# Kernel optimization log

Measured on AMD Instinct MI355X. Metric: run time of the kernel, lower is better.

## Reference

```python
import jax, jax.numpy as jnp
import numpy as np

N = 100000
E = 1600000
D_IN = 128
D_HID = 128

def setup_inputs() -> dict:
    key = jax.random.key(0)
    ks = jax.random.split(key, 8)
    x = jax.random.normal(ks[0], (N, D_IN), dtype=jnp.float32)
    edge_index = jax.random.randint(ks[1], (2, E), 0, N, dtype=jnp.int32)
    edge_weight = jax.random.uniform(ks[2], (E,), dtype=jnp.float32)
    W1 = jax.random.normal(ks[3], (D_IN, D_HID), dtype=jnp.float32) / np.sqrt(D_IN)
    b1 = jnp.zeros((D_HID,), dtype=jnp.float32)
    W2 = jax.random.normal(ks[4], (D_HID, D_HID), dtype=jnp.float32) / np.sqrt(D_HID)
    b2 = jnp.zeros((D_HID,), dtype=jnp.float32)
    W3 = jax.random.normal(ks[5], (D_HID, 1), dtype=jnp.float32) / np.sqrt(D_HID)
    b3 = jnp.zeros((1,), dtype=jnp.float32)
    return {"x": x, "edge_index": edge_index, "edge_weight": edge_weight,
            "W1": W1, "b1": b1, "W2": W2, "b2": b2, "W3": W3, "b3": b3}

def _gcn_norm(edge_index, edge_weight, n):
    # Add self-loops (weight 1) and compute symmetric normalization, as in PyG GCNConv.
    loop = jnp.arange(n, dtype=edge_index.dtype)
    src = jnp.concatenate([edge_index[0], loop])
    dst = jnp.concatenate([edge_index[1], loop])
    w = jnp.concatenate([edge_weight, jnp.ones((n,), edge_weight.dtype)])
    deg = jax.ops.segment_sum(w, dst, num_segments=n)  # [N]
    dis = jnp.where(deg > 0, jax.lax.rsqrt(jnp.where(deg > 0, deg, 1.0)), 0.0)
    norm = dis[src] * w * dis[dst]  # [E+N]
    return src, dst, norm

def _gcn_conv(x, W, b, src, dst, norm, n):
    h = x @ W  # [N, out]
    msg = norm[:, None] * h[src]  # gather + scale, [E+N, out]
    out = jax.ops.segment_sum(msg, dst, num_segments=n)  # scatter-add
    return out + b

def reference(x, edge_index, edge_weight, W1, b1, W2, b2, W3, b3):
    n = x.shape[0]
    src, dst, norm = _gcn_norm(edge_index, edge_weight, n)
    h = jax.nn.relu(_gcn_conv(x, W1, b1, src, dst, norm, n))
    h = jax.nn.relu(_gcn_conv(h, W2, b2, src, dst, norm, n))
    h = _gcn_conv(h, W3, b3, src, dst, norm, n)
    return jax.nn.relu(h).squeeze(-1)  # [N]
```

## Files before the change

### kernel.cpp

```cpp
#include <hip/hip_runtime.h>
#include <hip/hip_fp16.h>
#include <math.h>

#define NFEAT 128
#define CAP 64
#define BINSHIFT 7
#define GB 256

typedef int2 EdgeRec;

__device__ inline float4 h4_to_f4(uint2 u) {
  __half2 lo = *(__half2*)&u.x;
  __half2 hi = *(__half2*)&u.y;
  float2 a = __half22float2(lo), b = __half22float2(hi);
  return make_float4(a.x, a.y, b.x, b.y);
}
__device__ inline uint2 f4_to_h4(float4 v) {
  __half2 lo = __floats2half2_rn(v.x, v.y);
  __half2 hi = __floats2half2_rn(v.z, v.w);
  uint2 r; r.x = *(unsigned*)&lo; r.y = *(unsigned*)&hi; return r;
}


__global__ __launch_bounds__(256) void k_hist(const int* __restrict__ dst,
                                              unsigned* __restrict__ histG,
                                              int E, int EPB, int nbins) {
  __shared__ unsigned lh[1024];
  for (int i = threadIdx.x; i < nbins; i += 256) lh[i] = 0;
  __syncthreads();
  int start = blockIdx.x * EPB;
  int end = start + EPB; if (end > E) end = E;
  for (int e = start + threadIdx.x; e < end; e += 256)
    atomicAdd(&lh[dst[e] >> BINSHIFT], 1u);
  __syncthreads();
  for (int i = threadIdx.x; i < nbins; i += 256)
    histG[(size_t)i * GB + blockIdx.x] = lh[i];
}

__global__ __launch_bounds__(256) void k_scanT(const unsigned* __restrict__ histG,
                                               unsigned* __restrict__ binTot, int nbins) {
  int wave = threadIdx.x >> 6;
  int lane = threadIdx.x & 63;
  int bin = blockIdx.x * 4 + wave;
  if (bin >= nbins) return;
  uint4 v = *(const uint4*)(histG + (size_t)bin * GB + lane * 4);
  int s = (int)(v.x + v.y + v.z + v.w);
#pragma unroll
  for (int off = 32; off > 0; off >>= 1) s += __shfl_down(s, off, 64);
  if (lane == 0) binTot[bin] = (unsigned)s;
}

__global__ __launch_bounds__(1024) void k_scanB(const unsigned* __restrict__ binTot,
                                                unsigned* __restrict__ binBase, int nbins) {
  __shared__ unsigned tot[1024];
  int b = threadIdx.x;
  tot[b] = (b < nbins) ? binTot[b] : 0;
  __syncthreads();
  for (int off = 1; off < 1024; off <<= 1) {
    unsigned v = (b >= off) ? tot[b - off] : 0;
    __syncthreads();
    tot[b] += v;
    __syncthreads();
  }
  if (b < nbins) binBase[b] = (b == 0) ? 0u : tot[b - 1];
  if (b == 0) binBase[nbins] = tot[1023];
}

__global__ __launch_bounds__(256) void k_scanC(unsigned* __restrict__ histG,
                                               const unsigned* __restrict__ binBase,
                                               int nbins) {
  int wave = threadIdx.x >> 6;
  int lane = threadIdx.x & 63;
  int bin = blockIdx.x * 4 + wave;
  if (bin >= nbins) return;
  uint4 v = *(const uint4*)(histG + (size_t)bin * GB + lane * 4);
  unsigned i1 = v.x + v.y;
  unsigned i2 = i1 + v.z;
  unsigned i3 = i2 + v.w;
  int inc = (int)i3;
#pragma unroll
  for (int off = 1; off < 64; off <<= 1) {
    int t = __shfl_up(inc, off, 64);
    if (lane >= off) inc += t;
  }
  unsigned base = binBase[bin] + (unsigned)inc - i3;
  uint4 o;
  o.x = base;
  o.y = base + v.x;
  o.z = base + i1;
  o.w = base + i2;
  *(uint4*)(histG + (size_t)bin * GB + lane * 4) = o;
}

__global__ __launch_bounds__(256) void k_scatter(const int* __restrict__ src,
                                                 const int* __restrict__ dst,
                                                 const float* __restrict__ ew,
                                                 const unsigned* __restrict__ histG,
                                                 uint2* __restrict__ sorted,
                                                 int E, int EPB, int nbins) {
  __shared__ unsigned lrank[1024];
  __shared__ unsigned lbase[1024];
  for (int i = threadIdx.x; i < nbins; i += 256) {
    lrank[i] = 0;
    lbase[i] = histG[(size_t)i * GB + blockIdx.x];
  }
  __syncthreads();
  int start = blockIdx.x * EPB;
  int end = start + EPB; if (end > E) end = E;
  for (int e = start + threadIdx.x; e < end; e += 256) {
    int d = dst[e];
    int bin = d >> BINSHIFT;
    unsigned r = atomicAdd(&lrank[bin], 1u);
    uint2 rec;
    rec.x = (unsigned)src[e] | ((unsigned)(d & 127) << 24);
    rec.y = __float_as_uint(ew[e]);
    sorted[lbase[bin] + r] = rec;
  }
}

__global__ __launch_bounds__(256) void k_csr(const uint2* __restrict__ sorted,
                                             const unsigned* __restrict__ binBase,
                                             unsigned* __restrict__ cnt,
                                             EdgeRec* __restrict__ ep,
                                             float* __restrict__ dis, int N) {
  int bin = blockIdx.x;
  __shared__ unsigned lcnt[128];
  __shared__ float lsum[128];
  if (threadIdx.x < 128) { lcnt[threadIdx.x] = 0; lsum[threadIdx.x] = 0.f; }
  __syncthreads();
  unsigned s0 = binBase[bin], s1 = binBase[bin + 1];
  int node0 = bin << BINSHIFT;
  for (unsigned e = s0 + threadIdx.x; e < s1; e += 256) {
    uint2 rec = sorted[e];
    int dlow = rec.x >> 24;
    int srcn = rec.x & 0xFFFFFF;
    unsigned slot = atomicAdd(&lcnt[dlow], 1u);
    EdgeRec r; r.x = srcn; r.y = (int)rec.y;
    ep[(size_t)(node0 + dlow) * CAP + slot] = r;
    atomicAdd(&lsum[dlow], __uint_as_float(rec.y));
  }
  __syncthreads();
  if (threadIdx.x < 128) {
    int node = node0 + threadIdx.x;
    if (node < N) {
      cnt[node] = lcnt[threadIdx.x];
      dis[node] = 1.0f / sqrtf(1.0f + lsum[threadIdx.x]);
    }
  }
}

__global__ __launch_bounds__(256) void k_premul(EdgeRec* __restrict__ ep,
                                                const unsigned* __restrict__ cnt,
                                                const float* __restrict__ dis, int N) {
  int wave = threadIdx.x >> 6;
  int lane = threadIdx.x & 63;
  int node = blockIdx.x * 4 + wave;
  if (node >= N) return;
  int c = (int)cnt[node];
  if (lane < c) {
    int e = node * CAP + lane;
    EdgeRec r = ep[e];
    r.y = __float_as_int(dis[r.x] * __int_as_float(r.y));
    ep[e] = r;
  }
}


__global__ __launch_bounds__(1024) void k_gemm1(const float* __restrict__ X,
                                                const float* __restrict__ W,
                                                __half* __restrict__ Y,
                                                int N, int numTiles) {
  __shared__ float sW[128 * 128];
  __shared__ float sX[128 * 128];
  int t = threadIdx.x;
  int wave = __builtin_amdgcn_readfirstlane(t >> 6);
  int lane = t & 63;
  int lr = (lane >> 3) & 7;
  int lc = lane & 7;
  int wr = wave >> 2;
  int wc = wave & 3;

  {
    const float4* W4 = (const float4*)W;
    float4* sW4 = (float4*)sW;
    for (int i = t; i < 4096; i += 1024) sW4[i] = W4[i];
  }

  const float4* X4 = (const float4*)X;
  int grmax = N - 1;
  int r0 = wr * 32 + lr * 4;
  int c0 = wc * 32 + lc * 4;
  int swzk = ((r0 >> 2) & 7) << 2;

  for (int tile = blockIdx.x; tile < numTiles; tile += gridDim.x) {
    int rowBase = tile * 128;
    __syncthreads();
    {
      int kg = t & 31;
      int rb = t >> 5;
#pragma unroll
      for (int p = 0; p < 4; p++) {
        int r = rb + 32 * p;
        int gr = rowBase + r; if (gr > grmax) gr = grmax;
        float4 v = X4[(size_t)gr * 32 + kg];
        int swz = ((r >> 2) & 7) << 2;
        *(float4*)(&sX[r * 128 + ((kg * 4) ^ swz)]) = v;
      }
    }
    __syncthreads();

    float4 acc[4];
#pragma unroll
    for (int i = 0; i < 4; i++) acc[i] = make_float4(0.f, 0.f, 0.f, 0.f);

#pragma unroll 1
    for (int kg = 0; kg < 32; kg++) {
      int kk0 = kg * 4;
      float4 xf[4];
#pragma unroll
      for (int i = 0; i < 4; i++)
        xf[i] = *(const float4*)(&sX[(r0 + i) * 128 + (kk0 ^ swzk)]);
      float4 wf[4];
#pragma unroll
      for (int kk = 0; kk < 4; kk++)
        wf[kk] = *(const float4*)(&sW[(kk0 + kk) * 128 + c0]);
#pragma unroll
      for (int kk = 0; kk < 4; kk++) {
#pragma unroll
        for (int i = 0; i < 4; i++) {
          float xs = (&xf[i].x)[kk];
          acc[i].x = fmaf(xs, wf[kk].x, acc[i].x);
          acc[i].y = fmaf(xs, wf[kk].y, acc[i].y);
          acc[i].z = fmaf(xs, wf[kk].z, acc[i].z);
          acc[i].w = fmaf(xs, wf[kk].w, acc[i].w);
        }
      }
    }

#pragma unroll
    for (int i = 0; i < 4; i++) {
      int row = rowBase + r0 + i;
      if (row < N)
        *(uint2*)(Y + (size_t)row * 128 + c0) = f4_to_h4(acc[i]);
    }
  }
}


__global__ __launch_bounds__(1024) void k_aggemm(const __half* __restrict__ H,
                                                 const unsigned* __restrict__ cntA,
                                                 const EdgeRec* __restrict__ ep,
                                                 const float* __restrict__ dis,
                                                 const float* __restrict__ bias,
                                                 const float* __restrict__ Wm,
                                                 __half* __restrict__ Y,
                                                 int N, int numTiles) {
  __shared__ float sW[128 * 128];
  __shared__ float sX[2][64 * 128];
  int t = threadIdx.x;
  int wave = __builtin_amdgcn_readfirstlane(t >> 6);
  int lane = t & 63;

  {
    const float4* W4 = (const float4*)Wm;
    float4* sW4 = (float4*)sW;
    for (int i = t; i < 4096; i += 1024) sW4[i] = W4[i];
  }
  __syncthreads();

  int gw = wave;
  int half = lane >> 5;
  int l32 = lane & 31;
  int mw = wave - 12;
  int wr = (mw >> 1) & 1;
  int wc = mw & 1;
  int lr = (lane >> 3) & 7;
  int lc = lane & 7;
  int rB = wr * 32 + lr * 4;
  int cA = wc * 64 + lc * 4;
  int cB = cA + 32;
  int swzm = lr << 2;
  int s2b = 2 * gw;

  for (int it = 0;; it++) {
    int gtile = blockIdx.x + it * gridDim.x;
    int mtile = gtile - (int)gridDim.x;
    bool anyG = gtile < numTiles;
    bool anyM = (it >= 1) && (mtile < numTiles);
    if (!anyG && !anyM) break;

    if (wave < 12) {
      if (anyG) {
        float* buf = sX[it & 1];
        int tileBase = gtile * 64;
        int cnts[3];
#pragma unroll
        for (int k = 0; k < 3; k++) {
          int s2 = s2b + 24 * k;
          int node = tileBase + s2 + half;
          int nodec = node < N ? node : N - 1;
          unsigned pk = cntA[nodec];
          cnts[k] = (s2 < 64 && node < N) ? (int)pk : 0;
        }
#pragma unroll 1
        for (int k = 0; k < 3; k++) {
          int s2 = s2b + 24 * k;
          if (s2 >= 64) break;
          int node = tileBase + s2 + half;
          int cnt = cnts[k];
          int beg = (node < N ? node : 0) * CAP;
          int last = beg + cnt - 1;

          float4 acc = make_float4(0.f, 0.f, 0.f, 0.f);
          if (cnt > 0) {
            EdgeRec e0[4], e1[4], e2[4], e3[4];
            uint2 h0[4], h1[4];
#pragma unroll
            for (int q = 0; q < 4; q++) { int e = beg + q;     e0[q] = ep[e <= last ? e : last]; }
#pragma unroll
            for (int q = 0; q < 4; q++) { int e = beg + 4 + q; e1[q] = ep[e <= last ? e : last]; }
#pragma unroll
            for (int q = 0; q < 4; q++) { int e = beg + 8 + q; e2[q] = ep[e <= last ? e : last]; }
#pragma unroll
            for (int q = 0; q < 4; q++)
              h0[q] = *(const uint2*)(H + (size_t)e0[q].x * 128 + 4 * l32);
#pragma unroll
            for (int q = 0; q < 4; q++)
              h1[q] = *(const uint2*)(H + (size_t)e1[q].x * 128 + 4 * l32);
            for (int p = 0; p < cnt; p += 4) {
              uint2 h2[4];
#pragma unroll
              for (int q = 0; q < 4; q++) {
                int e = beg + p + 12 + q;
                e3[q] = ep[e <= last ? e : last];
              }
#pragma unroll
              for (int q = 0; q < 4; q++)
                h2[q] = *(const uint2*)(H + (size_t)e2[q].x * 128 + 4 * l32);
#pragma unroll
              for (int q = 0; q < 4; q++) {
                float w = (p + q < cnt) ? __int_as_float(e0[q].y) : 0.f;
                float4 hv = h4_to_f4(h0[q]);
                acc.x = fmaf(w, hv.x, acc.x);
                acc.y = fmaf(w, hv.y, acc.y);
                acc.z = fmaf(w, hv.z, acc.z);
                acc.w = fmaf(w, hv.w, acc.w);
              }
#pragma unroll
              for (int q = 0; q < 4; q++) {
                e0[q] = e1[q]; e1[q] = e2[q]; e2[q] = e3[q];
                h0[q] = h1[q]; h1[q] = h2[q];
              }
            }
          }
          if (node < N) {
            float ds = dis[node];
            float4 hn = h4_to_f4(*(const uint2*)(H + (size_t)node * 128 + 4 * l32));
            acc.x = fmaf(ds, hn.x, acc.x);
            acc.y = fmaf(ds, hn.y, acc.y);
            acc.z = fmaf(ds, hn.z, acc.z);
            acc.w = fmaf(ds, hn.w, acc.w);
            float4 bv = *(const float4*)(bias + 4 * l32);
            float4 o;
            o.x = fmaf(ds, acc.x, bv.x); o.x = o.x > 0.f ? o.x : 0.f;
            o.y = fmaf(ds, acc.y, bv.y); o.y = o.y > 0.f ? o.y : 0.f;
            o.z = fmaf(ds, acc.z, bv.z); o.z = o.z > 0.f ? o.z : 0.f;
            o.w = fmaf(ds, acc.w, bv.w); o.w = o.w > 0.f ? o.w : 0.f;
            int s = s2 + half;
            int swz = ((s >> 2) & 7) << 2;
            *(float4*)(&buf[s * 128 + ((4 * l32) ^ swz)]) = o;
          }
        }
      }
    } else {
      if (anyM) {
        const float* buf = sX[(it - 1) & 1];
        float4 accA[4], accB[4];
#pragma unroll
        for (int i = 0; i < 4; i++) {
          accA[i] = make_float4(0.f, 0.f, 0.f, 0.f);
          accB[i] = make_float4(0.f, 0.f, 0.f, 0.f);
        }
#pragma unroll 2
        for (int kg = 0; kg < 32; kg++) {
          int kk0 = kg * 4;
          float4 xf[4];
#pragma unroll
          for (int i = 0; i < 4; i++)
            xf[i] = *(const float4*)(&buf[(rB + i) * 128 + (kk0 ^ swzm)]);
#pragma unroll
          for (int kk = 0; kk < 4; kk++) {
            float4 wA = *(const float4*)(&sW[(kk0 + kk) * 128 + cA]);
            float4 wB = *(const float4*)(&sW[(kk0 + kk) * 128 + cB]);
#pragma unroll
            for (int i = 0; i < 4; i++) {
              float xs = (&xf[i].x)[kk];
              accA[i].x = fmaf(xs, wA.x, accA[i].x);
              accA[i].y = fmaf(xs, wA.y, accA[i].y);
              accA[i].z = fmaf(xs, wA.z, accA[i].z);
              accA[i].w = fmaf(xs, wA.w, accA[i].w);
              accB[i].x = fmaf(xs, wB.x, accB[i].x);
              accB[i].y = fmaf(xs, wB.y, accB[i].y);
              accB[i].z = fmaf(xs, wB.z, accB[i].z);
              accB[i].w = fmaf(xs, wB.w, accB[i].w);
            }
          }
        }
        int rowBase = mtile * 64;
#pragma unroll
        for (int i = 0; i < 4; i++) {
          int row = rowBase + rB + i;
          if (row < N) {
            *(uint2*)(Y + (size_t)row * 128 + cA) = f4_to_h4(accA[i]);
            *(uint2*)(Y + (size_t)row * 128 + cB) = f4_to_h4(accB[i]);
          }
        }
      }
    }
    __syncthreads();
  }
}


__global__ __launch_bounds__(256) void k_agg_final(const __half* __restrict__ H,
                                                   const unsigned* __restrict__ cntA,
                                                   const EdgeRec* __restrict__ ep,
                                                   const float* __restrict__ dis,
                                                   const float* __restrict__ bias,
                                                   const float* __restrict__ W3,
                                                   float* __restrict__ z, int N) {
  int wave = __builtin_amdgcn_readfirstlane(threadIdx.x >> 6);
  int lane = threadIdx.x & 63;
  int half = lane >> 5;
  int l32  = lane & 31;
  int node = blockIdx.x * 8 + wave * 2 + half;
  int nodec = node < N ? node : N - 1;
  int cnt = (node < N) ? (int)cntA[nodec] : 0;
  int beg = nodec * CAP;
  int last = beg + cnt - 1;

  float4 acc = make_float4(0.f, 0.f, 0.f, 0.f);
  if (cnt > 0) {
    EdgeRec e0[4], e1[4], e2[4];
    uint2 h0[4], h1[4];
#pragma unroll
    for (int q = 0; q < 4; q++) { int e = beg + q;     e0[q] = ep[e <= last ? e : last]; }
#pragma unroll
    for (int q = 0; q < 4; q++) { int e = beg + 4 + q; e1[q] = ep[e <= last ? e : last]; }
#pragma unroll
    for (int q = 0; q < 4; q++)
      h0[q] = *(const uint2*)(H + (size_t)e0[q].x * 128 + 4 * l32);
    for (int p = 0; p < cnt; p += 4) {
      uint2 h1n[4];
#pragma unroll
      for (int q = 0; q < 4; q++) {
        int e = beg + p + 8 + q;
        e2[q] = ep[e <= last ? e : last];
      }
#pragma unroll
      for (int q = 0; q < 4; q++)
        h1n[q] = *(const uint2*)(H + (size_t)e1[q].x * 128 + 4 * l32);
#pragma unroll
      for (int q = 0; q < 4; q++) {
        float w = (p + q < cnt) ? __int_as_float(e0[q].y) : 0.f;
        float4 hv = h4_to_f4(h0[q]);
        acc.x = fmaf(w, hv.x, acc.x);
        acc.y = fmaf(w, hv.y, acc.y);
        acc.z = fmaf(w, hv.z, acc.z);
        acc.w = fmaf(w, hv.w, acc.w);
      }
#pragma unroll
      for (int q = 0; q < 4; q++) { e0[q] = e1[q]; e1[q] = e2[q]; h0[q] = h1n[q]; }
    }
  }
  float ds = dis[nodec];
  float4 hn = h4_to_f4(*(const uint2*)(H + (size_t)nodec * 128 + 4 * l32));
  acc.x = fmaf(ds, hn.x, acc.x);
  acc.y = fmaf(ds, hn.y, acc.y);
  acc.z = fmaf(ds, hn.z, acc.z);
  acc.w = fmaf(ds, hn.w, acc.w);
  float4 bv = *(const float4*)(bias + 4 * l32);
  float4 w3v = *(const float4*)(W3 + 4 * l32);
  float o, pdot = 0.f;
  o = fmaf(ds, acc.x, bv.x); o = o > 0.f ? o : 0.f; pdot = fmaf(o, w3v.x, pdot);
  o = fmaf(ds, acc.y, bv.y); o = o > 0.f ? o : 0.f; pdot = fmaf(o, w3v.y, pdot);
  o = fmaf(ds, acc.z, bv.z); o = o > 0.f ? o : 0.f; pdot = fmaf(o, w3v.z, pdot);
  o = fmaf(ds, acc.w, bv.w); o = o > 0.f ? o : 0.f; pdot = fmaf(o, w3v.w, pdot);
#pragma unroll
  for (int off = 16; off > 0; off >>= 1) pdot += __shfl_down(pdot, off, 32);
  if (l32 == 0 && node < N) z[node] = pdot;
}


__global__ void k_aggs(const float* __restrict__ z, const unsigned* __restrict__ cntA,
                       const EdgeRec* __restrict__ ep, const float* __restrict__ dis,
                       const float* __restrict__ b3, float* __restrict__ out, int N) {
  int n = blockIdx.x * blockDim.x + threadIdx.x;
  if (n >= N) return;
  int cnt = (int)cntA[n];
  float dsn = dis[n];
  float acc = dsn * z[n];
  int beg = n * CAP;
#pragma unroll 4
  for (int e = beg; e < beg + cnt; e++) {
    EdgeRec p = ep[e];
    acc = fmaf(__int_as_float(p.y), z[p.x], acc);
  }
  acc = fmaf(dsn, acc, b3[0]);
  out[n] = acc > 0.f ? acc : 0.f;
}


extern "C" void kernel_launch(void* const* d_in, const int* in_sizes, int n_in,
                              void* d_out, int out_size, void* d_ws, size_t ws_size,
                              hipStream_t stream) {
  const float* x  = (const float*)d_in[0];
  const int*   ei = (const int*)d_in[1];
  const float* ew = (const float*)d_in[2];
  const float* W1 = (const float*)d_in[3];
  const float* b1 = (const float*)d_in[4];
  const float* W2 = (const float*)d_in[5];
  const float* b2 = (const float*)d_in[6];
  const float* W3 = (const float*)d_in[7];
  const float* b3 = (const float*)d_in[8];
  int N = in_sizes[0] / NFEAT;
  int E = in_sizes[2];
  const int* srcp = ei;
  const int* dstp = ei + E;

  char* p = (char*)d_ws;
  auto carve = [&](size_t bytes) -> void* {
    void* r = (void*)p;
    p += (bytes + 511) & ~(size_t)511;
    return r;
  };
  int nbins = (N + 127) >> BINSHIFT;
  unsigned* cnt     = (unsigned*)carve(sizeof(unsigned) * N);
  float*    dis     = (float*)carve(sizeof(float) * N);
  EdgeRec*  ep      = (EdgeRec*)carve(sizeof(EdgeRec) * (size_t)N * CAP);
  __half*   t1      = (__half*)carve(sizeof(__half) * (size_t)N * NFEAT);
  __half*   t2      = (__half*)carve(sizeof(__half) * (size_t)N * NFEAT);
  float*    z       = (float*)carve(sizeof(float) * N);
  unsigned* histG   = (unsigned*)carve(sizeof(unsigned) * (size_t)GB * nbins);
  unsigned* binTot  = (unsigned*)carve(sizeof(unsigned) * nbins);
  unsigned* binBase = (unsigned*)carve(sizeof(unsigned) * (nbins + 1));
  uint2*    sorted  = (uint2*)carve(sizeof(uint2) * (size_t)E);

  int gN = (N + 255) / 256;
  int numTiles128 = (N + 127) / 128;
  int numTiles64  = (N + 63) / 64;
  int GG = 256;
  int EPB = (E + GB - 1) / GB;
  int gS = (nbins + 3) / 4;
  int gP = (N + 3) / 4;
  int gF = (N + 7) / 8;

  k_hist<<<GB, 256, 0, stream>>>(dstp, histG, E, EPB, nbins);
  k_scanT<<<gS, 256, 0, stream>>>(histG, binTot, nbins);
  k_scanB<<<1, 1024, 0, stream>>>(binTot, binBase, nbins);
  k_scanC<<<gS, 256, 0, stream>>>(histG, binBase, nbins);
  k_scatter<<<GB, 256, 0, stream>>>(srcp, dstp, ew, histG, sorted, E, EPB, nbins);
  k_csr<<<nbins, 256, 0, stream>>>(sorted, binBase, cnt, ep, dis, N);
  k_gemm1<<<GG, 1024, 0, stream>>>(x, W1, t1, N, numTiles128);
  k_premul<<<gP, 256, 0, stream>>>(ep, cnt, dis, N);
  k_aggemm<<<GG, 1024, 0, stream>>>(t1, cnt, ep, dis, b1, W2, t2, N, numTiles64);
  k_agg_final<<<gF, 256, 0, stream>>>(t2, cnt, ep, dis, b2, W3, z, N);
  k_aggs<<<gN, 256, 0, stream>>>(z, cnt, ep, dis, b3, (float*)d_out, N);
}
```

Baseline: 430.7 us.

## Split each node's edge list across both wave halves and zero-pad CSR slots

The aggregation in k_aggemm and k_agg_final now gives each node one full wave instead of one half-wave. Each 32-lane half handles alternate edges, and the halves combine their partial sums with a cross-half shuffle. k_csr now zero-fills the unused slots in each node's fixed-capacity edge block so the loops can read padded entries safely without per-edge masking, and it clamps counts at CAP. This doubles the memory-level parallelism per node and lowers the per-wave edge-chain latency. The costs are extra zero-fill writes (about N*CAP records) during CSR construction, reduced work per wave, and a changed launch grid for the final aggregation.

```diff
diff --git a/kernel.cpp b/kernel.cpp
--- a/kernel.cpp
+++ b/kernel.cpp
@@ -135,15 +135,28 @@
     int dlow = rec.x >> 24;
     int srcn = rec.x & 0xFFFFFF;
     unsigned slot = atomicAdd(&lcnt[dlow], 1u);
-    EdgeRec r; r.x = srcn; r.y = (int)rec.y;
-    ep[(size_t)(node0 + dlow) * CAP + slot] = r;
+    if (slot < CAP) {
+      EdgeRec r; r.x = srcn; r.y = (int)rec.y;
+      ep[(size_t)(node0 + dlow) * CAP + slot] = r;
+    }
     atomicAdd(&lsum[dlow], __uint_as_float(rec.y));
   }
   __syncthreads();
+  for (int i = threadIdx.x; i < 128 * CAP; i += 256) {
+    int dlow = i >> 6;
+    int slot = i & (CAP - 1);
+    int node = node0 + dlow;
+    unsigned c = lcnt[dlow]; if (c > CAP) c = CAP;
+    if (node < N && (unsigned)slot >= c) {
+      EdgeRec zr; zr.x = 0; zr.y = 0;
+      ep[(size_t)node * CAP + slot] = zr;
+    }
+  }
   if (threadIdx.x < 128) {
     int node = node0 + threadIdx.x;
     if (node < N) {
-      cnt[node] = lcnt[threadIdx.x];
+      unsigned c = lcnt[threadIdx.x]; if (c > CAP) c = CAP;
+      cnt[node] = c;
       dis[node] = 1.0f / sqrtf(1.0f + lsum[threadIdx.x]);
     }
   }
@@ -269,7 +282,7 @@
   __syncthreads();
 
   int gw = wave;
-  int half = lane >> 5;
+  int hi = lane >> 5;
   int l32 = lane & 31;
   int mw = wave - 12;
   int wr = (mw >> 1) & 1;
@@ -280,7 +293,6 @@
   int cA = wc * 64 + lc * 4;
   int cB = cA + 32;
   int swzm = lr << 2;
-  int s2b = 2 * gw;
 
   for (int it = 0;; it++) {
     int gtile = blockIdx.x + it * gridDim.x;
@@ -293,67 +305,56 @@
       if (anyG) {
         float* buf = sX[it & 1];
         int tileBase = gtile * 64;
-        int cnts[3];
-#pragma unroll
-        for (int k = 0; k < 3; k++) {
-          int s2 = s2b + 24 * k;
-          int node = tileBase + s2 + half;
-          int nodec = node < N ? node : N - 1;
-          unsigned pk = cntA[nodec];
-          cnts[k] = (s2 < 64 && node < N) ? (int)pk : 0;
-        }
-#pragma unroll 1
-        for (int k = 0; k < 3; k++) {
-          int s2 = s2b + 24 * k;
-          if (s2 >= 64) break;
-          int node = tileBase + s2 + half;
-          int cnt = cnts[k];
-          int beg = (node < N ? node : 0) * CAP;
-          int last = beg + cnt - 1;
+        for (int s = gw; s < 64; s += 12) {
+          int node = tileBase + s;
+          if (node >= N) continue;
+          int cnt = (int)cntA[node];
+          int beg = node * CAP;
+          int emax = beg + CAP - 1;
 
           float4 acc = make_float4(0.f, 0.f, 0.f, 0.f);
           if (cnt > 0) {
-            EdgeRec e0[4], e1[4], e2[4], e3[4];
-            uint2 h0[4], h1[4];
-#pragma unroll
-            for (int q = 0; q < 4; q++) { int e = beg + q;     e0[q] = ep[e <= last ? e : last]; }
-#pragma unroll
-            for (int q = 0; q < 4; q++) { int e = beg + 4 + q; e1[q] = ep[e <= last ? e : last]; }
-#pragma unroll
-            for (int q = 0; q < 4; q++) { int e = beg + 8 + q; e2[q] = ep[e <= last ? e : last]; }
-#pragma unroll
-            for (int q = 0; q < 4; q++)
-              h0[q] = *(const uint2*)(H + (size_t)e0[q].x * 128 + 4 * l32);
-#pragma unroll
-            for (int q = 0; q < 4; q++)
-              h1[q] = *(const uint2*)(H + (size_t)e1[q].x * 128 + 4 * l32);
+            EdgeRec e0[4], e1[4];
+            uint2 hA0, hB0;
+#define LDE(d_, idx_) { int q_ = beg + (idx_); q_ = q_ <= emax ? q_ : emax; d_ = ep[q_]; }
+            LDE(e0[0], 0) LDE(e0[1], 1) LDE(e0[2], 2) LDE(e0[3], 3)
+            LDE(e1[0], 4) LDE(e1[1], 5) LDE(e1[2], 6) LDE(e1[3], 7)
+            {
+              int sA = hi ? e0[1].x : e0[0].x;
+              int sB = hi ? e0[3].x : e0[2].x;
+              hA0 = *(const uint2*)(H + (size_t)sA * 128 + 4 * l32);
+              hB0 = *(const uint2*)(H + (size_t)sB * 128 + 4 * l32);
+            }
             for (int p = 0; p < cnt; p += 4) {
-              uint2 h2[4];
-#pragma unroll
-              for (int q = 0; q < 4; q++) {
-                int e = beg + p + 12 + q;
-                e3[q] = ep[e <= last ? e : last];
-              }
-#pragma unroll
-              for (int q = 0; q < 4; q++)
-                h2[q] = *(const uint2*)(H + (size_t)e2[q].x * 128 + 4 * l32);
-#pragma unroll
-              for (int q = 0; q < 4; q++) {
-                float w = (p + q < cnt) ? __int_as_float(e0[q].y) : 0.f;
-                float4 hv = h4_to_f4(h0[q]);
-                acc.x = fmaf(w, hv.x, acc.x);
-                acc.y = fmaf(w, hv.y, acc.y);
-                acc.z = fmaf(w, hv.z, acc.z);
-                acc.w = fmaf(w, hv.w, acc.w);
-              }
-#pragma unroll
-              for (int q = 0; q < 4; q++) {
-                e0[q] = e1[q]; e1[q] = e2[q]; e2[q] = e3[q];
-                h0[q] = h1[q]; h1[q] = h2[q];
-              }
+              EdgeRec e2[4];
+              LDE(e2[0], p + 8) LDE(e2[1], p + 9) LDE(e2[2], p + 10) LDE(e2[3], p + 11)
+              int nA = hi ? e1[1].x : e1[0].x;
+              int nB = hi ? e1[3].x : e1[2].x;
+              uint2 hA1 = *(const uint2*)(H + (size_t)nA * 128 + 4 * l32);
+              uint2 hB1 = *(const uint2*)(H + (size_t)nB * 128 + 4 * l32);
+              float wA = __int_as_float(hi ? e0[1].y : e0[0].y);
+              float wB = __int_as_float(hi ? e0[3].y : e0[2].y);
+              float4 a = h4_to_f4(hA0);
+              float4 b = h4_to_f4(hB0);
+              acc.x = fmaf(wA, a.x, acc.x);
+              acc.y = fmaf(wA, a.y, acc.y);
+              acc.z = fmaf(wA, a.z, acc.z);
+              acc.w = fmaf(wA, a.w, acc.w);
+              acc.x = fmaf(wB, b.x, acc.x);
+              acc.y = fmaf(wB, b.y, acc.y);
+              acc.z = fmaf(wB, b.z, acc.z);
+              acc.w = fmaf(wB, b.w, acc.w);
+#pragma unroll
+              for (int q = 0; q < 4; q++) { e0[q] = e1[q]; e1[q] = e2[q]; }
+              hA0 = hA1; hB0 = hB1;
             }
+#undef LDE
           }
-          if (node < N) {
+          acc.x += __shfl_xor(acc.x, 32, 64);
+          acc.y += __shfl_xor(acc.y, 32, 64);
+          acc.z += __shfl_xor(acc.z, 32, 64);
+          acc.w += __shfl_xor(acc.w, 32, 64);
+          if (hi == 0) {
             float ds = dis[node];
             float4 hn = h4_to_f4(*(const uint2*)(H + (size_t)node * 128 + 4 * l32));
             acc.x = fmaf(ds, hn.x, acc.x);
@@ -366,7 +367,6 @@
             o.y = fmaf(ds, acc.y, bv.y); o.y = o.y > 0.f ? o.y : 0.f;
             o.z = fmaf(ds, acc.z, bv.z); o.z = o.z > 0.f ? o.z : 0.f;
             o.w = fmaf(ds, acc.w, bv.w); o.w = o.w > 0.f ? o.w : 0.f;
-            int s = s2 + half;
             int swz = ((s >> 2) & 7) << 2;
             *(float4*)(&buf[s * 128 + ((4 * l32) ^ swz)]) = o;
           }
@@ -431,64 +431,74 @@
                                                    float* __restrict__ z, int N) {
   int wave = __builtin_amdgcn_readfirstlane(threadIdx.x >> 6);
   int lane = threadIdx.x & 63;
-  int half = lane >> 5;
-  int l32  = lane & 31;
-  int node = blockIdx.x * 8 + wave * 2 + half;
-  int nodec = node < N ? node : N - 1;
-  int cnt = (node < N) ? (int)cntA[nodec] : 0;
-  int beg = nodec * CAP;
-  int last = beg + cnt - 1;
+  int hi = lane >> 5;
+  int l32 = lane & 31;
+  int node = blockIdx.x * 4 + wave;
+  if (node >= N) return;
+  int cnt = (int)cntA[node];
+  int beg = node * CAP;
+  int emax = beg + CAP - 1;
 
   float4 acc = make_float4(0.f, 0.f, 0.f, 0.f);
   if (cnt > 0) {
-    EdgeRec e0[4], e1[4], e2[4];
-    uint2 h0[4], h1[4];
-#pragma unroll
-    for (int q = 0; q < 4; q++) { int e = beg + q;     e0[q] = ep[e <= last ? e : last]; }
-#pragma unroll
-    for (int q = 0; q < 4; q++) { int e = beg + 4 + q; e1[q] = ep[e <= last ? e : last]; }
-#pragma unroll
-    for (int q = 0; q < 4; q++)
-      h0[q] = *(const uint2*)(H + (size_t)e0[q].x * 128 + 4 * l32);
+    EdgeRec e0[4], e1[4];
+    uint2 hA0, hB0;
+#define LDE(d_, idx_) { int q_ = beg + (idx_); q_ = q_ <= emax ? q_ : emax; d_ = ep[q_]; }
+    LDE(e0[0], 0) LDE(e0[1], 1) LDE(e0[2], 2) LDE(e0[3], 3)
+    LDE(e1[0], 4) LDE(e1[1], 5) LDE(e1[2], 6) LDE(e1[3], 7)
+    {
+      int sA = hi ? e0[1].x : e0[0].x;
+      int sB = hi ? e0[3].x : e0[2].x;
+      hA0 = *(const uint2*)(H + (size_t)sA * 128 + 4 * l32);
+      hB0 = *(const uint2*)(H + (size_t)sB * 128 + 4 * l32);
+    }
     for (int p = 0; p < cnt; p += 4) {
-      uint2 h1n[4];
-#pragma unroll
-      for (int q = 0; q < 4; q++) {
-        int e = beg + p + 8 + q;
-        e2[q] = ep[e <= last ? e : last];
-      }
-#pragma unroll
-      for (int q = 0; q < 4; q++)
-        h1n[q] = *(const uint2*)(H + (size_t)e1[q].x * 128 + 4 * l32);
-#pragma unroll
-      for (int q = 0; q < 4; q++) {
-        float w = (p + q < cnt) ? __int_as_float(e0[q].y) : 0.f;
-        float4 hv = h4_to_f4(h0[q]);
-        acc.x = fmaf(w, hv.x, acc.x);
-        acc.y = fmaf(w, hv.y, acc.y);
-        acc.z = fmaf(w, hv.z, acc.z);
-        acc.w = fmaf(w, hv.w, acc.w);
-      }
-#pragma unroll
-      for (int q = 0; q < 4; q++) { e0[q] = e1[q]; e1[q] = e2[q]; h0[q] = h1n[q]; }
-    }
-  }
-  float ds = dis[nodec];
-  float4 hn = h4_to_f4(*(const uint2*)(H + (size_t)nodec * 128 + 4 * l32));
-  acc.x = fmaf(ds, hn.x, acc.x);
-  acc.y = fmaf(ds, hn.y, acc.y);
-  acc.z = fmaf(ds, hn.z, acc.z);
-  acc.w = fmaf(ds, hn.w, acc.w);
-  float4 bv = *(const float4*)(bias + 4 * l32);
-  float4 w3v = *(const float4*)(W3 + 4 * l32);
-  float o, pdot = 0.f;
-  o = fmaf(ds, acc.x, bv.x); o = o > 0.f ? o : 0.f; pdot = fmaf(o, w3v.x, pdot);
-  o = fmaf(ds, acc.y, bv.y); o = o > 0.f ? o : 0.f; pdot = fmaf(o, w3v.y, pdot);
-  o = fmaf(ds, acc.z, bv.z); o = o > 0.f ? o : 0.f; pdot = fmaf(o, w3v.z, pdot);
-  o = fmaf(ds, acc.w, bv.w); o = o > 0.f ? o : 0.f; pdot = fmaf(o, w3v.w, pdot);
-#pragma unroll
-  for (int off = 16; off > 0; off >>= 1) pdot += __shfl_down(pdot, off, 32);
-  if (l32 == 0 && node < N) z[node] = pdot;
+      EdgeRec e2[4];
+      LDE(e2[0], p + 8) LDE(e2[1], p + 9) LDE(e2[2], p + 10) LDE(e2[3], p + 11)
+      int nA = hi ? e1[1].x : e1[0].x;
+      int nB = hi ? e1[3].x : e1[2].x;
+      uint2 hA1 = *(const uint2*)(H + (size_t)nA * 128 + 4 * l32);
+      uint2 hB1 = *(const uint2*)(H + (size_t)nB * 128 + 4 * l32);
+      float wA = __int_as_float(hi ? e0[1].y : e0[0].y);
+      float wB = __int_as_float(hi ? e0[3].y : e0[2].y);
+      float4 a = h4_to_f4(hA0);
+      float4 b = h4_to_f4(hB0);
+      acc.x = fmaf(wA, a.x, acc.x);
+      acc.y = fmaf(wA, a.y, acc.y);
+      acc.z = fmaf(wA, a.z, acc.z);
+      acc.w = fmaf(wA, a.w, acc.w);
+      acc.x = fmaf(wB, b.x, acc.x);
+      acc.y = fmaf(wB, b.y, acc.y);
+      acc.z = fmaf(wB, b.z, acc.z);
+      acc.w = fmaf(wB, b.w, acc.w);
+#pragma unroll
+      for (int q = 0; q < 4; q++) { e0[q] = e1[q]; e1[q] = e2[q]; }
+      hA0 = hA1; hB0 = hB1;
+    }
+#undef LDE
+  }
+  acc.x += __shfl_xor(acc.x, 32, 64);
+  acc.y += __shfl_xor(acc.y, 32, 64);
+  acc.z += __shfl_xor(acc.z, 32, 64);
+  acc.w += __shfl_xor(acc.w, 32, 64);
+  if (hi == 0) {
+    float ds = dis[node];
+    float4 hn = h4_to_f4(*(const uint2*)(H + (size_t)node * 128 + 4 * l32));
+    acc.x = fmaf(ds, hn.x, acc.x);
+    acc.y = fmaf(ds, hn.y, acc.y);
+    acc.z = fmaf(ds, hn.z, acc.z);
+    acc.w = fmaf(ds, hn.w, acc.w);
+    float4 bv = *(const float4*)(bias + 4 * l32);
+    float4 w3v = *(const float4*)(W3 + 4 * l32);
+    float o, pdot = 0.f;
+    o = fmaf(ds, acc.x, bv.x); o = o > 0.f ? o : 0.f; pdot = fmaf(o, w3v.x, pdot);
+    o = fmaf(ds, acc.y, bv.y); o = o > 0.f ? o : 0.f; pdot = fmaf(o, w3v.y, pdot);
+    o = fmaf(ds, acc.z, bv.z); o = o > 0.f ? o : 0.f; pdot = fmaf(o, w3v.z, pdot);
+    o = fmaf(ds, acc.w, bv.w); o = o > 0.f ? o : 0.f; pdot = fmaf(o, w3v.w, pdot);
+#pragma unroll
+    for (int off = 16; off > 0; off >>= 1) pdot += __shfl_down(pdot, off, 32);
+    if (l32 == 0) z[node] = pdot;
+  }
 }
 
 
@@ -537,7 +547,7 @@
   int nbins = (N + 127) >> BINSHIFT;
   unsigned* cnt     = (unsigned*)carve(sizeof(unsigned) * N);
   float*    dis     = (float*)carve(sizeof(float) * N);
-  EdgeRec*  ep      = (EdgeRec*)carve(sizeof(EdgeRec) * (size_t)N * CAP);
+  EdgeRec*  ep      = (EdgeRec*)carve(sizeof(EdgeRec) * ((size_t)N * CAP + 64));
   __half*   t1      = (__half*)carve(sizeof(__half) * (size_t)N * NFEAT);
   __half*   t2      = (__half*)carve(sizeof(__half) * (size_t)N * NFEAT);
   float*    z       = (float*)carve(sizeof(float) * N);
@@ -553,7 +563,6 @@
   int EPB = (E + GB - 1) / GB;
   int gS = (nbins + 3) / 4;
   int gP = (N + 3) / 4;
-  int gF = (N + 7) / 8;
 
   k_hist<<<GB, 256, 0, stream>>>(dstp, histG, E, EPB, nbins);
   k_scanT<<<gS, 256, 0, stream>>>(histG, binTot, nbins);
@@ -564,6 +573,6 @@
   k_gemm1<<<GG, 1024, 0, stream>>>(x, W1, t1, N, numTiles128);
   k_premul<<<gP, 256, 0, stream>>>(ep, cnt, dis, N);
   k_aggemm<<<GG, 1024, 0, stream>>>(t1, cnt, ep, dis, b1, W2, t2, N, numTiles64);
-  k_agg_final<<<gF, 256, 0, stream>>>(t2, cnt, ep, dis, b2, W3, z, N);
+  k_agg_final<<<gP, 256, 0, stream>>>(t2, cnt, ep, dis, b2, W3, z, N);
   k_aggs<<<gN, 256, 0, stream>>>(z, cnt, ep, dis, b3, (float*)d_out, N);
 }
```

Result: slower. 452.8 us (+5.1%).
